# Kernel tuning notes

Hardware: AMD Instinct MI355X
Metric: run time of the kernel (lower is better)

The kernel has to match this reference:

```python
import jax, jax.numpy as jnp
import numpy as np

M, K, N = 4096, 4096, 4096

def setup_inputs() -> dict:
    key = jax.random.key(0)
    k1, k2, k3 = jax.random.split(key, 3)
    a = jax.random.randint(k1, (M, K), 0, 127, dtype=jnp.int32)
    b = jax.random.randint(k2, (K, N), 0, 127, dtype=jnp.int32)
    scale = jax.random.uniform(k3, (N,), dtype=jnp.float32)
    return {"a": a, "b": b, "scale": scale}

def reference(a, b, scale):
    a8 = a.astype(jnp.int8)
    b8 = b.astype(jnp.int8)
    acc = jnp.matmul(a8, b8, preferred_element_type=jnp.int32)  # [M, N] int32
    # fused per-column (per-output-channel) dequantization scale
    return acc.astype(jnp.float32) * scale[None, :]  # [M, N] float32
```

## Files before the change

kernel.cpp:

```cpp
#include <hip/hip_runtime.h>
#include <stdint.h>

#define M_DIM 4096
#define K_DIM 4096
#define N_DIM 4096

typedef int v4i __attribute__((ext_vector_type(4)));
typedef int int32x4 __attribute__((ext_vector_type(4)));

__device__ __forceinline__ void gload_lds16(const void* g, void* l) {
    __builtin_amdgcn_global_load_lds(
        (const __attribute__((address_space(1))) uint32_t*)g,
        (__attribute__((address_space(3))) uint32_t*)l, 16, 0, 0);
}

__global__ void pack_ab_kernel(const int* __restrict__ a, char* __restrict__ a8,
                               const int* __restrict__ b, char* __restrict__ b8t) {
    __shared__ char tile[64][68];
    if (blockIdx.x < 2048) {
        int idx = blockIdx.x * 256 + threadIdx.x;
        const int stride = 2048 * 256;
        const int total4 = M_DIM * K_DIM / 4;
        for (int i = idx; i < total4; i += stride) {
            int32x4 v = ((const int32x4*)a)[i];
            uint32_t p = (uint32_t)(v.x & 0xff) | ((uint32_t)(v.y & 0xff) << 8) |
                         ((uint32_t)(v.z & 0xff) << 16) | ((uint32_t)(v.w & 0xff) << 24);
            ((uint32_t*)a8)[i] = p;
        }
    } else {
        int bid2 = blockIdx.x - 2048;
        int n0 = (bid2 & 63) * 64;
        int k0 = (bid2 >> 6) * 64;
        int tx = threadIdx.x & 63;
        int ty = threadIdx.x >> 6;
#pragma unroll
        for (int kk = 0; kk < 64; kk += 4) {
            tile[kk + ty][tx] = (char)b[(size_t)(k0 + kk + ty) * N_DIM + n0 + tx];
        }
        __syncthreads();
        int td = threadIdx.x & 15;
        int tn = threadIdx.x >> 4;
#pragma unroll
        for (int nn0 = 0; nn0 < 64; nn0 += 16) {
            int nn = nn0 + tn;
            uint32_t p = (uint32_t)(uint8_t)tile[td * 4 + 0][nn] |
                         ((uint32_t)(uint8_t)tile[td * 4 + 1][nn] << 8) |
                         ((uint32_t)(uint8_t)tile[td * 4 + 2][nn] << 16) |
                         ((uint32_t)(uint8_t)tile[td * 4 + 3][nn] << 24);
            *(uint32_t*)&b8t[(size_t)(n0 + nn) * K_DIM + k0 + td * 4] = p;
        }
    }
}

#define BM 256
#define BN 256
#define KTILES (K_DIM / 64)

#define BAR __builtin_amdgcn_s_barrier()
#define WAIT_VM4 asm volatile("s_waitcnt vmcnt(4)" ::: "memory")
#define WAIT_VM0 asm volatile("s_waitcnt vmcnt(0)" ::: "memory")
#define WAIT_LGKM0 asm volatile("s_waitcnt lgkmcnt(0)" ::: "memory")

#define RD_FRAGS(RA, RB)                                                                \
    _Pragma("unroll") for (int i_ = 0; i_ < 8; ++i_)                                    \
        RA[i_] = *(const v4i*)(lds + nxt + aOff + i_ * 1024);                           \
    _Pragma("unroll") for (int j_ = 0; j_ < 4; ++j_)                                    \
        RB[j_] = *(const v4i*)(lds + nxt + bOff + j_ * 1024);

#define SGB_HINT                                                                        \
    _Pragma("unroll") for (int g_ = 0; g_ < 12; ++g_) {                                 \
        __builtin_amdgcn_sched_group_barrier(0x100, 1, 0);               \
        __builtin_amdgcn_sched_group_barrier(0x008, 2, 0);                  \
    }                                                                                   \
    __builtin_amdgcn_sched_group_barrier(0x008, 8, 0);

#define MFMA32(AF, BF)                                                                  \
    __builtin_amdgcn_s_setprio(1);                                                      \
    _Pragma("unroll") for (int i_ = 0; i_ < 8; ++i_)                                    \
    _Pragma("unroll") for (int j_ = 0; j_ < 4; ++j_)                                    \
        acc[i_][j_] = __builtin_amdgcn_mfma_i32_16x16x64_i8(AF[i_], BF[j_],             \
                                                            acc[i_][j_], 0, 0, 0);     \
    __builtin_amdgcn_s_setprio(0);

#define WINDOW(w, RA, RB, MA, MB)                                                       \
    {                                                                                   \
        stage((w) + 2, stg);                                                            \
        WAIT_VM4;                                                                       \
        BAR;                                                                            \
        RD_FRAGS(RA, RB);                                                               \
        SGB_HINT;                                                                       \
        MFMA32(MA, MB);                                                                 \
        WAIT_LGKM0;                                                                     \
        int t_ = cur; cur = nxt; nxt = stg; stg = t_;                                   \
    }

__global__ __launch_bounds__(512, 2) void gemm_i8_pp(const char* __restrict__ A8,
                                                     const char* __restrict__ B8T,
                                                     const float* __restrict__ scale,
                                                     float* __restrict__ out) {
    __shared__ char lds[98304];

    int tid = threadIdx.x;
    int wave = tid >> 6;
    int lane = tid & 63;
    int wr = wave >> 2;
    int wc = wave & 3;
    int l15 = lane & 15;

    int bid = blockIdx.x;
    int swz = (bid & 7) * 32 + (bid >> 3);
    int bm = swz >> 4;
    int bn = swz & 15;

    int rA = tid >> 2;
    int cc = ((tid & 3) ^ ((tid >> 3) & 3)) << 4;
    const char* aSrc = A8 + (size_t)(bm * BM + rA) * K_DIM + cc;
    const char* bSrc = B8T + (size_t)(bn * BN + rA) * K_DIM + cc;

    int slot = (((lane >> 4) ^ ((lane >> 1) & 3)) << 4);
    int aOff = wr * 8192 + l15 * 64 + slot;
    int bOff = 16384 + wc * 4096 + l15 * 64 + slot;

    v4i acc[8][4];
#pragma unroll
    for (int i = 0; i < 8; ++i)
#pragma unroll
        for (int j = 0; j < 4; ++j) acc[i][j] = (v4i){0, 0, 0, 0};

    auto stage = [&](int w, int bo) {
        const char* sa = aSrc + (size_t)w * 64;
        const char* sb = bSrc + (size_t)w * 64;
        char* da = (char*)lds + bo + wave * 1024;
        char* db = da + 16384;
        gload_lds16(sa, da);
        gload_lds16(sa + (size_t)128 * K_DIM, da + 8192);
        gload_lds16(sb, db);
        gload_lds16(sb + (size_t)128 * K_DIM, db + 8192);
    };

    stage(0, 0);
    stage(1, 32768);
    WAIT_VM4;
    BAR;

    int cur = 0, nxt = 32768, stg = 65536;
    v4i pA[8], pB[4], qA[8], qB[4];
    {
#pragma unroll
        for (int i = 0; i < 8; ++i) pA[i] = *(const v4i*)(lds + cur + aOff + i * 1024);
#pragma unroll
        for (int j = 0; j < 4; ++j) pB[j] = *(const v4i*)(lds + cur + bOff + j * 1024);
    }

    for (int kt = 0; kt < KTILES - 2; kt += 2) {
        WINDOW(kt, qA, qB, pA, pB);
        WINDOW(kt + 1, pA, pB, qA, qB);
    }

    WAIT_VM0;
    BAR;
    RD_FRAGS(qA, qB);
    MFMA32(pA, pB);
    MFMA32(qA, qB);

    size_t orow0 = (size_t)bm * BM + wr * 128 + (lane >> 4) * 4;
    int ocol0 = bn * BN + wc * 64 + l15;
#pragma unroll
    for (int j = 0; j < 4; ++j) {
        int col = ocol0 + j * 16;
        float s = scale[col];
#pragma unroll
        for (int i = 0; i < 8; ++i) {
            size_t row = orow0 + (size_t)i * 16;
#pragma unroll
            for (int r = 0; r < 4; ++r) {
                out[(row + r) * N_DIM + col] = (float)acc[i][j][r] * s;
            }
        }
    }
}

#define FBM 128
#define FBN 128
#define FBK 64

__global__ __launch_bounds__(256) void gemm_i8_fused_kernel(const int* __restrict__ a,
                                                            const int* __restrict__ b,
                                                            const float* __restrict__ scale,
                                                            float* __restrict__ out) {
    __shared__ char As[FBM * FBK];
    __shared__ char Bs[FBN * FBK];

    int tid = threadIdx.x;
    int wave = tid >> 6;
    int lane = tid & 63;

    int nwg = gridDim.x;
    int cpx = nwg >> 3;
    int bid = blockIdx.x;
    int swz = (bid & 7) * cpx + (bid >> 3);
    int bm = swz >> 5;
    int bn = swz & 31;

    int f0 = tid * 16;
    int m0 = f0 >> 6;
    int k0 = f0 & 63;

    int nn = tid & 127;
    int kh = tid >> 7;

    int wr = wave >> 1;
    int wc = wave & 1;
    int lrow = lane & 15;
    int kgrp = (lane >> 4) * 16;

    v4i acc[4][4];
#pragma unroll
    for (int i = 0; i < 4; ++i)
#pragma unroll
        for (int j = 0; j < 4; ++j) acc[i][j] = (v4i){0, 0, 0, 0};

    const int kTiles = K_DIM / FBK;
    for (int kt = 0; kt < kTiles; ++kt) {
        __syncthreads();
#pragma unroll
        for (int r = 0; r < 2; ++r) {
            const int* src = a + (size_t)(bm * FBM + m0 + r * 64) * K_DIM + kt * FBK + k0;
            uint32_t pk[4];
#pragma unroll
            for (int q = 0; q < 4; ++q) {
                int32x4 v = *(const int32x4*)(src + q * 4);
                pk[q] = (uint32_t)(v.x & 0xff) | ((uint32_t)(v.y & 0xff) << 8) |
                        ((uint32_t)(v.z & 0xff) << 16) | ((uint32_t)(v.w & 0xff) << 24);
            }
            *(v4i*)&As[f0 + r * 4096] = (v4i){(int)pk[0], (int)pk[1], (int)pk[2], (int)pk[3]};
        }
#pragma unroll
        for (int d = 0; d < 8; ++d) {
            uint32_t p = 0;
#pragma unroll
            for (int i = 0; i < 4; ++i) {
                int kk = kt * FBK + kh * 32 + d * 4 + i;
                p |= (uint32_t)(b[(size_t)kk * N_DIM + bn * FBN + nn] & 0xff) << (8 * i);
            }
            *(uint32_t*)&Bs[nn * 64 + kh * 32 + d * 4] = p;
        }
        __syncthreads();

        v4i aF[4], bF[4];
#pragma unroll
        for (int i = 0; i < 4; ++i)
            aF[i] = *(const v4i*)&As[(wr * 64 + i * 16 + lrow) * FBK + kgrp];
#pragma unroll
        for (int j = 0; j < 4; ++j)
            bF[j] = *(const v4i*)&Bs[(wc * 64 + j * 16 + lrow) * FBK + kgrp];
#pragma unroll
        for (int i = 0; i < 4; ++i)
#pragma unroll
            for (int j = 0; j < 4; ++j)
                acc[i][j] = __builtin_amdgcn_mfma_i32_16x16x64_i8(aF[i], bF[j], acc[i][j], 0, 0, 0);
    }

    size_t orow0 = (size_t)bm * FBM + wr * 64;
    int ocol0 = bn * FBN + wc * 64;
#pragma unroll
    for (int j = 0; j < 4; ++j) {
        int col = ocol0 + j * 16 + lrow;
        float s = scale[col];
#pragma unroll
        for (int i = 0; i < 4; ++i) {
            size_t row = orow0 + i * 16 + (lane >> 4) * 4;
#pragma unroll
            for (int r = 0; r < 4; ++r) {
                out[(row + r) * N_DIM + col] = (float)acc[i][j][r] * s;
            }
        }
    }
}

extern "C" void kernel_launch(void* const* d_in, const int* in_sizes, int n_in,
                              void* d_out, int out_size, void* d_ws, size_t ws_size,
                              hipStream_t stream) {
    const int* a = (const int*)d_in[0];
    const int* b = (const int*)d_in[1];
    const float* scale = (const float*)d_in[2];
    float* out = (float*)d_out;

    size_t need = (size_t)M_DIM * K_DIM + (size_t)K_DIM * N_DIM;
    if (ws_size >= need) {
        char* a8 = (char*)d_ws;
        char* b8t = a8 + (size_t)M_DIM * K_DIM;
        pack_ab_kernel<<<2048 + 4096, 256, 0, stream>>>(a, a8, b, b8t);
        gemm_i8_pp<<<256, 512, 0, stream>>>(a8, b8t, scale, out);
    } else {
        gemm_i8_fused_kernel<<<1024, 256, 0, stream>>>(a, b, scale, out);
    }
}
```

Measured before the change: 93.30 us.

## Switch int8 GEMM inner loop to 32x32x32 MFMA with remapped LDS fragments

Replaces the 16x16x64 int8 MFMA tiling with 32x32x32 instructions, so each wave issues 16 larger MFMAs per k-tile instead of 32 small ones and holds 4x2 v16i accumulators. LDS fragment addressing, swizzle slot and the output row mapping are rewritten to match the 32x32 layout, and the scheduling hints are adjusted. The aim is fewer MFMA issues and possibly better per-instruction throughput or operand reuse. The price is a different accumulator register layout and a riskier fragment-to-LDS mapping that could cause bank conflicts.

```diff
diff --git a/kernel.cpp b/kernel.cpp
--- a/kernel.cpp
+++ b/kernel.cpp
@@ -6,6 +6,7 @@
 #define N_DIM 4096
 
 typedef int v4i __attribute__((ext_vector_type(4)));
+typedef int v16i __attribute__((ext_vector_type(16)));
 typedef int int32x4 __attribute__((ext_vector_type(4)));
 
 __device__ __forceinline__ void gload_lds16(const void* g, void* l) {
@@ -62,39 +63,46 @@
 #define WAIT_LGKM0 asm volatile("s_waitcnt lgkmcnt(0)" ::: "memory")
 
 #define RD_FRAGS(RA, RB)                                                                \
-    _Pragma("unroll") for (int i_ = 0; i_ < 8; ++i_)                                    \
-        RA[i_] = *(const v4i*)(lds + nxt + aOff + i_ * 1024);                           \
-    _Pragma("unroll") for (int j_ = 0; j_ < 4; ++j_)                                    \
-        RB[j_] = *(const v4i*)(lds + nxt + bOff + j_ * 1024);
+    _Pragma("unroll") for (int m_ = 0; m_ < 4; ++m_)                                    \
+        RA[m_] = *(const v4i*)(lds + nxt + aOff + m_ * 2048);                           \
+    _Pragma("unroll") for (int m_ = 0; m_ < 4; ++m_)                                    \
+        RA[4 + m_] = *(const v4i*)(lds + nxt + ((aOff + m_ * 2048) ^ 32));              \
+    _Pragma("unroll") for (int n_ = 0; n_ < 2; ++n_)                                    \
+        RB[n_] = *(const v4i*)(lds + nxt + bOff + n_ * 2048);                           \
+    _Pragma("unroll") for (int n_ = 0; n_ < 2; ++n_)                                    \
+        RB[2 + n_] = *(const v4i*)(lds + nxt + ((bOff + n_ * 2048) ^ 32));
 
 #define SGB_HINT                                                                        \
-    _Pragma("unroll") for (int g_ = 0; g_ < 12; ++g_) {                                 \
+    __builtin_amdgcn_sched_group_barrier(0x100, 4, 0);                                  \
+    _Pragma("unroll") for (int g_ = 0; g_ < 8; ++g_) {                                  \
         __builtin_amdgcn_sched_group_barrier(0x100, 1, 0);               \
-        __builtin_amdgcn_sched_group_barrier(0x008, 2, 0);                  \
+        __builtin_amdgcn_sched_group_barrier(0x008, 1, 0);                  \
     }                                                                                   \
     __builtin_amdgcn_sched_group_barrier(0x008, 8, 0);
 
-#define MFMA32(AF, BF)                                                                  \
+#define MFMA16(AF, BF)                                                                  \
     __builtin_amdgcn_s_setprio(1);                                                      \
-    _Pragma("unroll") for (int i_ = 0; i_ < 8; ++i_)                                    \
-    _Pragma("unroll") for (int j_ = 0; j_ < 4; ++j_)                                    \
-        acc[i_][j_] = __builtin_amdgcn_mfma_i32_16x16x64_i8(AF[i_], BF[j_],             \
-                                                            acc[i_][j_], 0, 0, 0);     \
+    _Pragma("unroll") for (int k_ = 0; k_ < 2; ++k_)                                    \
+    _Pragma("unroll") for (int m_ = 0; m_ < 4; ++m_)                                    \
+    _Pragma("unroll") for (int n_ = 0; n_ < 2; ++n_)                                    \
+        acc[m_][n_] = __builtin_amdgcn_mfma_i32_32x32x32_i8(AF[k_ * 4 + m_],            \
+                                                            BF[k_ * 2 + n_],           \
+                                                            acc[m_][n_], 0, 0, 0);     \
     __builtin_amdgcn_s_setprio(0);
 
-#define WINDOW(w, RA, RB, MA, MB)                                                       \
+#define WINDOW(w, LA, LB, UA, UB)                                                       \
     {                                                                                   \
         stage((w) + 2, stg);                                                            \
         WAIT_VM4;                                                                       \
         BAR;                                                                            \
-        RD_FRAGS(RA, RB);                                                               \
+        RD_FRAGS(LA, LB);                                                               \
         SGB_HINT;                                                                       \
-        MFMA32(MA, MB);                                                                 \
+        MFMA16(UA, UB);                                                                 \
         WAIT_LGKM0;                                                                     \
         int t_ = cur; cur = nxt; nxt = stg; stg = t_;                                   \
     }
 
-__global__ __launch_bounds__(512, 2) void gemm_i8_pp(const char* __restrict__ A8,
+__global__ __launch_bounds__(512, 2) void gemm_i8_32(const char* __restrict__ A8,
                                                      const char* __restrict__ B8T,
                                                      const float* __restrict__ scale,
                                                      float* __restrict__ out) {
@@ -105,7 +113,8 @@
     int lane = tid & 63;
     int wr = wave >> 2;
     int wc = wave & 3;
-    int l15 = lane & 15;
+    int l31 = lane & 31;
+    int hi = lane >> 5;
 
     int bid = blockIdx.x;
     int swz = (bid & 7) * 32 + (bid >> 3);
@@ -117,15 +126,16 @@
     const char* aSrc = A8 + (size_t)(bm * BM + rA) * K_DIM + cc;
     const char* bSrc = B8T + (size_t)(bn * BN + rA) * K_DIM + cc;
 
-    int slot = (((lane >> 4) ^ ((lane >> 1) & 3)) << 4);
-    int aOff = wr * 8192 + l15 * 64 + slot;
-    int bOff = 16384 + wc * 4096 + l15 * 64 + slot;
-
-    v4i acc[8][4];
-#pragma unroll
-    for (int i = 0; i < 8; ++i)
-#pragma unroll
-        for (int j = 0; j < 4; ++j) acc[i][j] = (v4i){0, 0, 0, 0};
+    int xr = (l31 >> 1) & 3;
+    int slot = (hi ^ xr) << 4;
+    int aOff = wr * 8192 + l31 * 64 + slot;
+    int bOff = 16384 + wc * 4096 + l31 * 64 + slot;
+
+    v16i acc[4][2];
+#pragma unroll
+    for (int i = 0; i < 4; ++i)
+#pragma unroll
+        for (int j = 0; j < 2; ++j) acc[i][j] = (v16i)(0);
 
     auto stage = [&](int w, int bo) {
         const char* sa = aSrc + (size_t)w * 64;
@@ -147,9 +157,15 @@
     v4i pA[8], pB[4], qA[8], qB[4];
     {
 #pragma unroll
-        for (int i = 0; i < 8; ++i) pA[i] = *(const v4i*)(lds + cur + aOff + i * 1024);
-#pragma unroll
-        for (int j = 0; j < 4; ++j) pB[j] = *(const v4i*)(lds + cur + bOff + j * 1024);
+        for (int m = 0; m < 4; ++m) {
+            pA[m] = *(const v4i*)(lds + cur + aOff + m * 2048);
+            pA[4 + m] = *(const v4i*)(lds + cur + ((aOff + m * 2048) ^ 32));
+        }
+#pragma unroll
+        for (int n = 0; n < 2; ++n) {
+            pB[n] = *(const v4i*)(lds + cur + bOff + n * 2048);
+            pB[2 + n] = *(const v4i*)(lds + cur + ((bOff + n * 2048) ^ 32));
+        }
     }
 
     for (int kt = 0; kt < KTILES - 2; kt += 2) {
@@ -160,21 +176,23 @@
     WAIT_VM0;
     BAR;
     RD_FRAGS(qA, qB);
-    MFMA32(pA, pB);
-    MFMA32(qA, qB);
-
-    size_t orow0 = (size_t)bm * BM + wr * 128 + (lane >> 4) * 4;
-    int ocol0 = bn * BN + wc * 64 + l15;
-#pragma unroll
-    for (int j = 0; j < 4; ++j) {
-        int col = ocol0 + j * 16;
+    MFMA16(pA, pB);
+    WAIT_LGKM0;
+    MFMA16(qA, qB);
+
+    size_t orow0 = (size_t)bm * BM + wr * 128 + hi * 4;
+    int ocol0 = bn * BN + wc * 64 + l31;
+#pragma unroll
+    for (int nt = 0; nt < 2; ++nt) {
+        int col = ocol0 + nt * 32;
         float s = scale[col];
 #pragma unroll
-        for (int i = 0; i < 8; ++i) {
-            size_t row = orow0 + (size_t)i * 16;
-#pragma unroll
-            for (int r = 0; r < 4; ++r) {
-                out[(row + r) * N_DIM + col] = (float)acc[i][j][r] * s;
+        for (int mt = 0; mt < 4; ++mt) {
+            size_t rbase = orow0 + mt * 32;
+#pragma unroll
+            for (int reg = 0; reg < 16; ++reg) {
+                size_t row = rbase + (reg & 3) + 8 * (reg >> 2);
+                out[row * N_DIM + col] = (float)acc[mt][nt][reg] * s;
             }
         }
     }
@@ -291,7 +309,7 @@
         char* a8 = (char*)d_ws;
         char* b8t = a8 + (size_t)M_DIM * K_DIM;
         pack_ab_kernel<<<2048 + 4096, 256, 0, stream>>>(a, a8, b, b8t);
-        gemm_i8_pp<<<256, 512, 0, stream>>>(a8, b8t, scale, out);
+        gemm_i8_32<<<256, 512, 0, stream>>>(a8, b8t, scale, out);
     } else {
         gemm_i8_fused_kernel<<<1024, 256, 0, stream>>>(a, b, scale, out);
     }
```

Result: slower. 98.55 us (+5.6%).

## Fuse A int32-to-int8 packing into the GEMM mainloop via register staging

Applied to the files above, without the earlier changes.

Removes the separate pass that packs A into int8. The GEMM now loads A directly as int32 into registers, packs it to int8 and writes it to LDS after the MFMA block, while B is still pre-transposed and packed by a smaller kernel. This drops a full read and write of A from a standalone kernel. In exchange the GEMM fetches four times more A bytes per tile, much of it repeatedly across column blocks, and holds extra staging registers that raise VGPR pressure and may cause spills.

```diff
diff --git a/kernel.cpp b/kernel.cpp
--- a/kernel.cpp
+++ b/kernel.cpp
@@ -14,41 +14,27 @@
         (__attribute__((address_space(3))) uint32_t*)l, 16, 0, 0);
 }
 
-__global__ void pack_ab_kernel(const int* __restrict__ a, char* __restrict__ a8,
-                               const int* __restrict__ b, char* __restrict__ b8t) {
+__global__ void pack_bt_kernel(const int* __restrict__ b, char* __restrict__ b8t) {
     __shared__ char tile[64][68];
-    if (blockIdx.x < 2048) {
-        int idx = blockIdx.x * 256 + threadIdx.x;
-        const int stride = 2048 * 256;
-        const int total4 = M_DIM * K_DIM / 4;
-        for (int i = idx; i < total4; i += stride) {
-            int32x4 v = ((const int32x4*)a)[i];
-            uint32_t p = (uint32_t)(v.x & 0xff) | ((uint32_t)(v.y & 0xff) << 8) |
-                         ((uint32_t)(v.z & 0xff) << 16) | ((uint32_t)(v.w & 0xff) << 24);
-            ((uint32_t*)a8)[i] = p;
-        }
-    } else {
-        int bid2 = blockIdx.x - 2048;
-        int n0 = (bid2 & 63) * 64;
-        int k0 = (bid2 >> 6) * 64;
-        int tx = threadIdx.x & 63;
-        int ty = threadIdx.x >> 6;
-#pragma unroll
-        for (int kk = 0; kk < 64; kk += 4) {
-            tile[kk + ty][tx] = (char)b[(size_t)(k0 + kk + ty) * N_DIM + n0 + tx];
-        }
-        __syncthreads();
-        int td = threadIdx.x & 15;
-        int tn = threadIdx.x >> 4;
-#pragma unroll
-        for (int nn0 = 0; nn0 < 64; nn0 += 16) {
-            int nn = nn0 + tn;
-            uint32_t p = (uint32_t)(uint8_t)tile[td * 4 + 0][nn] |
-                         ((uint32_t)(uint8_t)tile[td * 4 + 1][nn] << 8) |
-                         ((uint32_t)(uint8_t)tile[td * 4 + 2][nn] << 16) |
-                         ((uint32_t)(uint8_t)tile[td * 4 + 3][nn] << 24);
-            *(uint32_t*)&b8t[(size_t)(n0 + nn) * K_DIM + k0 + td * 4] = p;
-        }
+    int k0 = blockIdx.y * 64;
+    int n0 = blockIdx.x * 64;
+    int tx = threadIdx.x & 63;
+    int ty = threadIdx.x >> 6;
+#pragma unroll
+    for (int kk = 0; kk < 64; kk += 4) {
+        tile[kk + ty][tx] = (char)b[(size_t)(k0 + kk + ty) * N_DIM + n0 + tx];
+    }
+    __syncthreads();
+    int td = threadIdx.x & 15;
+    int tn = threadIdx.x >> 4;
+#pragma unroll
+    for (int nn0 = 0; nn0 < 64; nn0 += 16) {
+        int nn = nn0 + tn;
+        uint32_t p = (uint32_t)(uint8_t)tile[td * 4 + 0][nn] |
+                     ((uint32_t)(uint8_t)tile[td * 4 + 1][nn] << 8) |
+                     ((uint32_t)(uint8_t)tile[td * 4 + 2][nn] << 16) |
+                     ((uint32_t)(uint8_t)tile[td * 4 + 3][nn] << 24);
+        *(uint32_t*)&b8t[(size_t)(n0 + nn) * K_DIM + k0 + td * 4] = p;
     }
 }
 
@@ -57,7 +43,8 @@
 #define KTILES (K_DIM / 64)
 
 #define BAR __builtin_amdgcn_s_barrier()
-#define WAIT_VM4 asm volatile("s_waitcnt vmcnt(4)" ::: "memory")
+#define WAIT_VM10 asm volatile("s_waitcnt vmcnt(10)" ::: "memory")
+#define WAIT_VM2 asm volatile("s_waitcnt vmcnt(2)" ::: "memory")
 #define WAIT_VM0 asm volatile("s_waitcnt vmcnt(0)" ::: "memory")
 #define WAIT_LGKM0 asm volatile("s_waitcnt lgkmcnt(0)" ::: "memory")
 
@@ -82,19 +69,22 @@
                                                             acc[i_][j_], 0, 0, 0);     \
     __builtin_amdgcn_s_setprio(0);
 
-#define WINDOW(w, RA, RB, MA, MB)                                                       \
+#define WINDOW_AF(w, RA, RB, MA, MB)                                                    \
     {                                                                                   \
-        stage((w) + 2, stg);                                                            \
-        WAIT_VM4;                                                                       \
+        loadA((w) + 2, rS);                                                             \
+        stageB((w) + 2, stg);                                                           \
+        WAIT_VM10;                                                                      \
         BAR;                                                                            \
         RD_FRAGS(RA, RB);                                                               \
         SGB_HINT;                                                                       \
         MFMA32(MA, MB);                                                                 \
+        __builtin_amdgcn_sched_barrier(0);                                              \
+        packWriteA(rS, stg);                                                            \
         WAIT_LGKM0;                                                                     \
         int t_ = cur; cur = nxt; nxt = stg; stg = t_;                                   \
     }
 
-__global__ __launch_bounds__(512, 2) void gemm_i8_pp(const char* __restrict__ A8,
+__global__ __launch_bounds__(512, 2) void gemm_i8_af(const int* __restrict__ A32,
                                                      const char* __restrict__ B8T,
                                                      const float* __restrict__ scale,
                                                      float* __restrict__ out) {
@@ -113,9 +103,9 @@
     int bn = swz & 15;
 
     int rA = tid >> 2;
-    int cc = ((tid & 3) ^ ((tid >> 3) & 3)) << 4;
-    const char* aSrc = A8 + (size_t)(bm * BM + rA) * K_DIM + cc;
-    const char* bSrc = B8T + (size_t)(bn * BN + rA) * K_DIM + cc;
+    int ck = (tid & 3) ^ ((tid >> 3) & 3);
+    const int* aSrcI = A32 + (size_t)(bm * BM + rA) * K_DIM + ck * 16;
+    const char* bSrc = B8T + (size_t)(bn * BN + rA) * K_DIM + ck * 16;
 
     int slot = (((lane >> 4) ^ ((lane >> 1) & 3)) << 4);
     int aOff = wr * 8192 + l15 * 64 + slot;
@@ -127,20 +117,44 @@
 #pragma unroll
         for (int j = 0; j < 4; ++j) acc[i][j] = (v4i){0, 0, 0, 0};
 
-    auto stage = [&](int w, int bo) {
-        const char* sa = aSrc + (size_t)w * 64;
+    auto stageB = [&](int w, int bo) {
         const char* sb = bSrc + (size_t)w * 64;
-        char* da = (char*)lds + bo + wave * 1024;
-        char* db = da + 16384;
-        gload_lds16(sa, da);
-        gload_lds16(sa + (size_t)128 * K_DIM, da + 8192);
+        char* db = (char*)lds + bo + 16384 + wave * 1024;
         gload_lds16(sb, db);
         gload_lds16(sb + (size_t)128 * K_DIM, db + 8192);
     };
-
-    stage(0, 0);
-    stage(1, 32768);
-    WAIT_VM4;
+    auto loadA = [&](int w, int32x4* r) {
+        const int* as = aSrcI + (size_t)w * 64;
+#pragma unroll
+        for (int q = 0; q < 4; ++q) r[q] = *(const int32x4*)(as + q * 4);
+        const int* as2 = as + (size_t)128 * K_DIM;
+#pragma unroll
+        for (int q = 0; q < 4; ++q) r[4 + q] = *(const int32x4*)(as2 + q * 4);
+    };
+    auto packWriteA = [&](const int32x4* r, int bo) {
+        uint32_t pk[8];
+#pragma unroll
+        for (int q = 0; q < 8; ++q) {
+            int32x4 v = r[q];
+            pk[q] = (uint32_t)(v.x & 0xff) | ((uint32_t)(v.y & 0xff) << 8) |
+                    ((uint32_t)(v.z & 0xff) << 16) | ((uint32_t)(v.w & 0xff) << 24);
+        }
+        *(v4i*)((char*)lds + bo + tid * 16) =
+            (v4i){(int)pk[0], (int)pk[1], (int)pk[2], (int)pk[3]};
+        *(v4i*)((char*)lds + bo + 8192 + tid * 16) =
+            (v4i){(int)pk[4], (int)pk[5], (int)pk[6], (int)pk[7]};
+    };
+
+    int32x4 rS[8], rT[8];
+
+    loadA(0, rS);
+    loadA(1, rT);
+    stageB(0, 0);
+    stageB(1, 32768);
+    packWriteA(rS, 0);
+    packWriteA(rT, 32768);
+    WAIT_VM2;
+    WAIT_LGKM0;
     BAR;
 
     int cur = 0, nxt = 32768, stg = 65536;
@@ -153,8 +167,8 @@
     }
 
     for (int kt = 0; kt < KTILES - 2; kt += 2) {
-        WINDOW(kt, qA, qB, pA, pB);
-        WINDOW(kt + 1, pA, pB, qA, qB);
+        WINDOW_AF(kt, qA, qB, pA, pB);
+        WINDOW_AF(kt + 1, pA, pB, qA, qB);
     }
 
     WAIT_VM0;
@@ -286,12 +300,11 @@
     const float* scale = (const float*)d_in[2];
     float* out = (float*)d_out;
 
-    size_t need = (size_t)M_DIM * K_DIM + (size_t)K_DIM * N_DIM;
+    size_t need = (size_t)K_DIM * N_DIM;
     if (ws_size >= need) {
-        char* a8 = (char*)d_ws;
-        char* b8t = a8 + (size_t)M_DIM * K_DIM;
-        pack_ab_kernel<<<2048 + 4096, 256, 0, stream>>>(a, a8, b, b8t);
-        gemm_i8_pp<<<256, 512, 0, stream>>>(a8, b8t, scale, out);
+        char* b8t = (char*)d_ws;
+        pack_bt_kernel<<<dim3(64, 64), 256, 0, stream>>>(b, b8t);
+        gemm_i8_af<<<256, 512, 0, stream>>>(a, b8t, scale, out);
     } else {
         gemm_i8_fused_kernel<<<1024, 256, 0, stream>>>(a, b, scale, out);
     }
```

Measured after the change: 154.5 us. +65.6%, slower.
